# Kernel tuning notes

Measured on AMD Instinct MI355X. Metric: run time of the kernel, lower is better.

The kernel has to match this reference:

```python
import jax, jax.numpy as jnp
import numpy as np

B, S, D, MEM, STRIDE = 8, 8192, 128, 128, 64

def setup_inputs() -> dict:
    key = jax.random.key(0)
    ks = jax.random.split(key, 6)
    scale = 0.01  # matches nn.init.normal_(w, 0.0, 0.01)
    x = jax.random.normal(ks[0], (B, S, D), dtype=jnp.float32)
    Wq = scale * jax.random.normal(ks[1], (D, D), dtype=jnp.float32)
    Wk = scale * jax.random.normal(ks[2], (D, D), dtype=jnp.float32)
    Wv = scale * jax.random.normal(ks[3], (MEM, D), dtype=jnp.float32)
    Wg_w = jnp.zeros((1, D), dtype=jnp.float32)       # W_g weight init zeros
    Wg_b = jnp.full((1,), -2.0, dtype=jnp.float32)    # W_g bias init -2.0
    Wout = scale * jax.random.normal(ks[4], (D, MEM), dtype=jnp.float32)
    return {"x": x, "Wq": Wq, "Wk": Wk, "Wv": Wv, "Wg_w": Wg_w, "Wg_b": Wg_b, "Wout": Wout}

def reference(x, Wq, Wk, Wv, Wg_w, Wg_b, Wout):
    b, s, d = x.shape
    nC = s // STRIDE  # S assumed divisible by stride
    q = x @ Wq.T                                  # [B,S,D]
    k = x @ Wk.T                                  # [B,S,D]
    v = x @ Wv.T                                  # [B,S,MEM]
    g = jax.nn.sigmoid(x @ Wg_w.T + Wg_b)         # [B,S,1]
    # chunk: leading scan axis nC
    qc = q.reshape(b, nC, STRIDE, d).transpose(1, 0, 2, 3)
    kc = k.reshape(b, nC, STRIDE, d).transpose(1, 0, 2, 3)
    vc = v.reshape(b, nC, STRIDE, MEM).transpose(1, 0, 2, 3)
    gc = g.reshape(b, nC, STRIDE, 1).transpose(1, 0, 2, 3)

    def step(M, chunk):
        qch, kch, vch, gch = chunk
        reads = jnp.einsum('bsd,bdm->bsm', qch, M)              # read before write
        write = jnp.einsum('bsd,bsm->bdm', kch * gch, vch)      # gated outer-product
        avg_gate = gch.mean(axis=1, keepdims=True)              # [B,1,1]
        M_new = (1.0 - avg_gate) * M + write
        return M_new, reads

    M0 = jnp.zeros((b, d, MEM), dtype=x.dtype)
    _, reads = jax.lax.scan(step, M0, (qc, kc, vc, gc))         # [nC,B,STRIDE,MEM]
    out = reads.transpose(1, 0, 2, 3).reshape(b, s, MEM)
    return out @ Wout.T                                         # [B,S,D]
```

## Files before the change

kernel.cpp:

```cpp
#include <hip/hip_runtime.h>

#define Bn 8
#define Sn 8192
#define Dn 128
#define NCn 128

typedef _Float16 f16;
typedef f16 f16x2 __attribute__((ext_vector_type(2)));
typedef f16 f16x4 __attribute__((ext_vector_type(4)));
typedef float f32x4 __attribute__((ext_vector_type(4)));

static __device__ __forceinline__ f32x4 mfma16(f16x4 a, f16x4 b, f32x4 c) {
  return __builtin_amdgcn_mfma_f32_16x16x16f16(a, b, c, 0, 0, 0);
}

union UU { uint4 u; f16x2 h[4]; f16x4 q[2]; };


__global__ __launch_bounds__(64) void k_prep(
    const float* __restrict__ Wq, const float* __restrict__ Wk,
    const float* __restrict__ Wv, const float* __restrict__ Wout,
    f16* __restrict__ Amat, f16* __restrict__ r2) {
  const int blk = blockIdx.x;
  const int which = blk >> 6;
  const int t = blk & 63, ti = t >> 3, tj = t & 7;
  const int lane = threadIdx.x & 63, r16 = lane & 15, g4 = lane >> 4;
  f32x4 acc = {};
  if (which == 0) {
#pragma unroll
    for (int kk = 0; kk < 8; ++kk) {
      f16x4 af, bf;
#pragma unroll
      for (int j = 0; j < 4; ++j) {
        af[j] = (f16)Wq[(kk * 16 + g4 * 4 + j) * 128 + ti * 16 + r16];
        bf[j] = (f16)Wk[(kk * 16 + g4 * 4 + j) * 128 + tj * 16 + r16];
      }
      acc = mfma16(af, bf, acc);
    }
  } else {
#pragma unroll
    for (int kk = 0; kk < 8; ++kk) {
      f16x4 af, bf;
      float4 a4 = *(const float4*)(Wout + (ti * 16 + r16) * 128 + kk * 16 + g4 * 4);
      af[0] = (f16)a4.x; af[1] = (f16)a4.y; af[2] = (f16)a4.z; af[3] = (f16)a4.w;
#pragma unroll
      for (int j = 0; j < 4; ++j)
        bf[j] = (f16)Wv[(kk * 16 + g4 * 4 + j) * 128 + tj * 16 + r16];
      acc = mfma16(af, bf, acc);
    }
  }
  f16* dst = which ? r2 : Amat;
#pragma unroll
  for (int j = 0; j < 4; ++j)
    dst[(ti * 16 + g4 * 4 + j) * 128 + tj * 16 + r16] = (f16)acc[j];
}

__global__ __launch_bounds__(512, 8) void k_phase1(
    const float* __restrict__ x, const float* __restrict__ gw, const float* __restrict__ gb,
    const f16* __restrict__ Amat, const f16* __restrict__ r2,
    f16x4* __restrict__ wtg, float* __restrict__ gavg, f16* __restrict__ xh) {
  __shared__ __align__(16) f16 Xs[64][136];
  __shared__ __align__(16) f16x4 vP[2048];
  __shared__ float gs[64];
  const int h = blockIdx.x;
  const int grp = h & 127, m = h >> 7;
  const int b = grp >> 4, seg = grp & 15;
  const int c = seg * 8 + m;
  const int tid = threadIdx.x;
  {
    int s = tid >> 3, sub = tid & 7;
    const float* xrow = x + ((size_t)b * Sn + (size_t)c * 64 + s) * Dn;
    f16* xhrow = xh + (size_t)(b * NCn + c) * 8192 + s * 128;
    float gpart = 0.f;
#pragma unroll
    for (int i = 0; i < 4; ++i) {
      int col = sub * 4 + i * 32;
      float4 v = *(const float4*)(xrow + col);
      float4 g = *(const float4*)(gw + col);
      gpart += v.x * g.x + v.y * g.y + v.z * g.z + v.w * g.w;
      f16x4 hh = {(f16)v.x, (f16)v.y, (f16)v.z, (f16)v.w};
      *(f16x4*)&Xs[s][col] = hh;
      *(f16x4*)&xhrow[col] = hh;
    }
    gpart += __shfl_xor(gpart, 1);
    gpart += __shfl_xor(gpart, 2);
    gpart += __shfl_xor(gpart, 4);
    if (sub == 0) gs[s] = 1.f / (1.f + __expf(-(gpart + gb[0])));
  }
  __syncthreads();
  if (tid == 0) {
    float sum = 0.f;
#pragma unroll
    for (int i = 0; i < 64; ++i) sum += gs[i];
    gavg[b * NCn + c] = sum * (1.f / 64.f);
  }
  const int w = tid >> 6, lane = tid & 63, r16 = lane & 15, g4 = lane >> 4;
  f32x4 uacc[4] = {}, vacc[4] = {};
#pragma unroll
  for (int kk = 0; kk < 8; ++kk) {
    f16x4 bu = *(const f16x4*)&Amat[(w * 16 + r16) * 128 + kk * 16 + g4 * 4];
    f16x4 bv = *(const f16x4*)&r2[(w * 16 + r16) * 128 + kk * 16 + g4 * 4];
#pragma unroll
    for (int mr = 0; mr < 4; ++mr) {
      f16x4 af = *(f16x4*)&Xs[mr * 16 + r16][kk * 16 + g4 * 4];
      uacc[mr] = mfma16(af, bu, uacc[mr]);
      vacc[mr] = mfma16(af, bv, vacc[mr]);
    }
  }
  f16x4 ua[4];
#pragma unroll
  for (int mr = 0; mr < 4; ++mr) {
    float g0 = gs[mr * 16 + g4 * 4 + 0], g1 = gs[mr * 16 + g4 * 4 + 1];
    float g2 = gs[mr * 16 + g4 * 4 + 2], g3 = gs[mr * 16 + g4 * 4 + 3];
    f16x4 uh = {(f16)(uacc[mr][0] * g0), (f16)(uacc[mr][1] * g1),
                (f16)(uacc[mr][2] * g2), (f16)(uacc[mr][3] * g3)};
    ua[mr] = uh;
    f16x4 vh = {(f16)vacc[mr][0], (f16)vacc[mr][1], (f16)vacc[mr][2], (f16)vacc[mr][3]};
    vP[(mr * 8 + w) * 64 + lane] = vh;
  }
  __syncthreads();
  f32x4 z[8] = {};
#pragma unroll
  for (int ks = 0; ks < 4; ++ks)
#pragma unroll
    for (int ct = 0; ct < 8; ++ct)
      z[ct] = mfma16(ua[ks], vP[(ks * 8 + ct) * 64 + lane], z[ct]);
  f16x4* wdst = wtg + (size_t)(b * NCn + c) * 4096;
#pragma unroll
  for (int ct = 0; ct < 8; ++ct) {
    f16x4 zh = {(f16)z[ct][0], (f16)z[ct][1], (f16)z[ct][2], (f16)z[ct][3]};
    wdst[(w * 8 + ct) * 64 + lane] = zh;
  }
}

__global__ __launch_bounds__(512, 4) void k_outfold(
    const f16* __restrict__ xh, const uint4* __restrict__ wtg4,
    const float* __restrict__ gavg, float* __restrict__ outp) {
  __shared__ __align__(16) f16 Xs[64][136];
  __shared__ __align__(16) float Mf[4096];
  __shared__ __align__(16) f16x4 Mh4[1024];
  const int blk = blockIdx.x;
  const int seg = 15 - (blk >> 5);
  const int sub5 = blk & 31;
  const int b = sub5 >> 2, q = sub5 & 3;
  const int tid = threadIdx.x;
  const int w = tid >> 6, lane = tid & 63, r16 = lane & 15, g4 = lane >> 4;
  const int mr = w & 3, tq = w >> 2;

  const int lt = tid >> 5;
  const int gtile = (lt >> 1) * 8 + q * 2 + (lt & 1);
  const int slot = tid & 31;

  float4 P0 = {0.f, 0.f, 0.f, 0.f}, P1 = {0.f, 0.f, 0.f, 0.f};
  {
    const uint4* Zb = wtg4 + (size_t)(b * NCn) * 2048 + gtile * 32 + slot;
    const float* ga = gavg + b * NCn;
    const int nt = seg * 8;
#pragma unroll 4
    for (int t = 0; t < nt; ++t) {
      UU z; z.u = Zb[(size_t)t * 2048];
      float dd = 1.f - ga[t];
      P0.x = dd * P0.x + (float)z.h[0][0];
      P0.y = dd * P0.y + (float)z.h[0][1];
      P0.z = dd * P0.z + (float)z.h[1][0];
      P0.w = dd * P0.w + (float)z.h[1][1];
      P1.x = dd * P1.x + (float)z.h[2][0];
      P1.y = dd * P1.y + (float)z.h[2][1];
      P1.z = dd * P1.z + (float)z.h[3][0];
      P1.w = dd * P1.w + (float)z.h[3][1];
    }
  }
  float4* Mf4 = (float4*)Mf;
  Mf4[tid * 2] = P0;
  Mf4[tid * 2 + 1] = P1;

  float dseg[8];
#pragma unroll
  for (int t = 0; t < 8; ++t) dseg[t] = 1.f - gavg[b * NCn + seg * 8 + t];

  const uint4* Zseg = wtg4 + (size_t)(b * NCn + seg * 8) * 2048;
  const f16* xhseg = xh + (size_t)(b * NCn + seg * 8) * 8192;
  const int xrow = tid >> 3, xcol = (tid & 7) * 16;

  uint4 xa = ((const uint4*)xhseg)[tid * 2];
  uint4 xb2 = ((const uint4*)xhseg)[tid * 2 + 1];

  for (int m = 0; m < 8; ++m) {
    *(uint4*)&Xs[xrow][xcol] = xa;
    *(uint4*)&Xs[xrow][xcol + 8] = xb2;
#pragma unroll
    for (int h2 = 0; h2 < 2; ++h2) {
      float4 mv = Mf4[tid * 2 + h2];
      f16x4 hh = {(f16)mv.x, (f16)mv.y, (f16)mv.z, (f16)mv.w};
      Mh4[tid * 2 + h2] = hh;
    }
    __syncthreads();

    UU z;
    z.u = Zseg[(size_t)m * 2048 + gtile * 32 + slot];
    if (m < 7) {
      const uint4* xn = (const uint4*)(xhseg + (size_t)(m + 1) * 8192);
      xa = xn[tid * 2];
      xb2 = xn[tid * 2 + 1];
    }

    f32x4 acc = {};
#pragma unroll
    for (int kk = 0; kk < 8; ++kk) {
      f16x4 af = *(f16x4*)&Xs[mr * 16 + r16][kk * 16 + g4 * 4];
      f16x4 bf = Mh4[(kk * 2 + tq) * 64 + lane];
      acc = mfma16(af, bf, acc);
    }

    {
      float dd = dseg[m];
#pragma unroll
      for (int h2 = 0; h2 < 2; ++h2) {
        float4 mv = Mf4[tid * 2 + h2];
        mv.x = dd * mv.x + (float)z.h[2 * h2][0];
        mv.y = dd * mv.y + (float)z.h[2 * h2][1];
        mv.z = dd * mv.z + (float)z.h[2 * h2 + 1][0];
        mv.w = dd * mv.w + (float)z.h[2 * h2 + 1][1];
        Mf4[tid * 2 + h2] = mv;
      }
    }

    {
      const int c = seg * 8 + m;
      float* ob = outp + ((size_t)b * Sn + (size_t)c * 64 + mr * 16 + g4 * 4) * Dn +
                  (q * 2 + tq) * 16 + r16;
#pragma unroll
      for (int j = 0; j < 4; ++j) ob[(size_t)j * Dn] = acc[j];
    }
    __syncthreads();
  }
}

extern "C" void kernel_launch(void* const* d_in, const int* in_sizes, int n_in,
                              void* d_out, int out_size, void* d_ws, size_t ws_size,
                              hipStream_t stream) {
  const float* x = (const float*)d_in[0];
  const float* Wq = (const float*)d_in[1];
  const float* Wk = (const float*)d_in[2];
  const float* Wv = (const float*)d_in[3];
  const float* gw = (const float*)d_in[4];
  const float* gb = (const float*)d_in[5];
  const float* Wout = (const float*)d_in[6];

  char* ws = (char*)d_ws;
  f16* Amat = (f16*)(ws + 0);
  f16* r2 = (f16*)(ws + 32768);
  float* gavg = (float*)(ws + 65536);
  f16* wtg = (f16*)(ws + 69632);
  f16* xh = (f16*)(ws + 37556224);

  k_prep<<<dim3(128), dim3(64), 0, stream>>>(Wq, Wk, Wv, Wout, Amat, r2);
  k_phase1<<<dim3(Bn * NCn), dim3(512), 0, stream>>>(x, gw, gb, Amat, r2, (f16x4*)wtg,
                                                     gavg, xh);
  k_outfold<<<dim3(512), dim3(512), 0, stream>>>(xh, (const uint4*)wtg, gavg,
                                                 (float*)d_out);
}
```

Measured before the change: 62.56 us.

## Keep memory state in registers and double-buffer shared tiles in outfold

```diff
diff --git a/kernel.cpp b/kernel.cpp
--- a/kernel.cpp
+++ b/kernel.cpp
@@ -17,13 +17,15 @@
 union UU { uint4 u; f16x2 h[4]; f16x4 q[2]; };
 
 
-__global__ __launch_bounds__(64) void k_prep(
+__global__ __launch_bounds__(256) void k_prep(
     const float* __restrict__ Wq, const float* __restrict__ Wk,
     const float* __restrict__ Wv, const float* __restrict__ Wout,
     f16* __restrict__ Amat, f16* __restrict__ r2) {
   const int blk = blockIdx.x;
-  const int which = blk >> 6;
-  const int t = blk & 63, ti = t >> 3, tj = t & 7;
+  const int which = blk >> 4;
+  const int w = threadIdx.x >> 6;
+  const int t = (blk & 15) * 4 + w;
+  const int ti = t >> 3, tj = t & 7;
   const int lane = threadIdx.x & 63, r16 = lane & 15, g4 = lane >> 4;
   f32x4 acc = {};
   if (which == 0) {
@@ -63,8 +65,7 @@
   __shared__ __align__(16) f16x4 vP[2048];
   __shared__ float gs[64];
   const int h = blockIdx.x;
-  const int grp = h & 127, m = h >> 7;
-  const int b = grp >> 4, seg = grp & 15;
+  const int b = h & 7, seg = (h >> 3) & 15, m = h >> 7;
   const int c = seg * 8 + m;
   const int tid = threadIdx.x;
   {
@@ -136,43 +137,36 @@
 __global__ __launch_bounds__(512, 4) void k_outfold(
     const f16* __restrict__ xh, const uint4* __restrict__ wtg4,
     const float* __restrict__ gavg, float* __restrict__ outp) {
-  __shared__ __align__(16) f16 Xs[64][136];
-  __shared__ __align__(16) float Mf[4096];
-  __shared__ __align__(16) f16x4 Mh4[1024];
+  __shared__ __align__(16) f16 Xs[2][64][136];
+  __shared__ __align__(16) f16x4 Mh4[2][1024];
   const int blk = blockIdx.x;
-  const int seg = 15 - (blk >> 5);
-  const int sub5 = blk & 31;
-  const int b = sub5 >> 2, q = sub5 & 3;
+  const int b = blk & 7, q = (blk >> 3) & 3, seg = 15 - (blk >> 5);
   const int tid = threadIdx.x;
   const int w = tid >> 6, lane = tid & 63, r16 = lane & 15, g4 = lane >> 4;
   const int mr = w & 3, tq = w >> 2;
-
   const int lt = tid >> 5;
   const int gtile = (lt >> 1) * 8 + q * 2 + (lt & 1);
   const int slot = tid & 31;
 
-  float4 P0 = {0.f, 0.f, 0.f, 0.f}, P1 = {0.f, 0.f, 0.f, 0.f};
+  float4 M0 = {0.f, 0.f, 0.f, 0.f}, M1 = {0.f, 0.f, 0.f, 0.f};
   {
     const uint4* Zb = wtg4 + (size_t)(b * NCn) * 2048 + gtile * 32 + slot;
     const float* ga = gavg + b * NCn;
     const int nt = seg * 8;
-#pragma unroll 4
+#pragma unroll 8
     for (int t = 0; t < nt; ++t) {
       UU z; z.u = Zb[(size_t)t * 2048];
       float dd = 1.f - ga[t];
-      P0.x = dd * P0.x + (float)z.h[0][0];
-      P0.y = dd * P0.y + (float)z.h[0][1];
-      P0.z = dd * P0.z + (float)z.h[1][0];
-      P0.w = dd * P0.w + (float)z.h[1][1];
-      P1.x = dd * P1.x + (float)z.h[2][0];
-      P1.y = dd * P1.y + (float)z.h[2][1];
-      P1.z = dd * P1.z + (float)z.h[3][0];
-      P1.w = dd * P1.w + (float)z.h[3][1];
-    }
-  }
-  float4* Mf4 = (float4*)Mf;
-  Mf4[tid * 2] = P0;
-  Mf4[tid * 2 + 1] = P1;
+      M0.x = dd * M0.x + (float)z.h[0][0];
+      M0.y = dd * M0.y + (float)z.h[0][1];
+      M0.z = dd * M0.z + (float)z.h[1][0];
+      M0.w = dd * M0.w + (float)z.h[1][1];
+      M1.x = dd * M1.x + (float)z.h[2][0];
+      M1.y = dd * M1.y + (float)z.h[2][1];
+      M1.z = dd * M1.z + (float)z.h[3][0];
+      M1.w = dd * M1.w + (float)z.h[3][1];
+    }
+  }
 
   float dseg[8];
 #pragma unroll
@@ -185,15 +179,14 @@
   uint4 xa = ((const uint4*)xhseg)[tid * 2];
   uint4 xb2 = ((const uint4*)xhseg)[tid * 2 + 1];
 
+#pragma unroll
   for (int m = 0; m < 8; ++m) {
-    *(uint4*)&Xs[xrow][xcol] = xa;
-    *(uint4*)&Xs[xrow][xcol + 8] = xb2;
-#pragma unroll
-    for (int h2 = 0; h2 < 2; ++h2) {
-      float4 mv = Mf4[tid * 2 + h2];
-      f16x4 hh = {(f16)mv.x, (f16)mv.y, (f16)mv.z, (f16)mv.w};
-      Mh4[tid * 2 + h2] = hh;
-    }
+    f16(*Xsb)[136] = Xs[m & 1];
+    f16x4* Mh = Mh4[m & 1];
+    *(uint4*)&Xsb[xrow][xcol] = xa;
+    *(uint4*)&Xsb[xrow][xcol + 8] = xb2;
+    Mh[tid * 2] = (f16x4){(f16)M0.x, (f16)M0.y, (f16)M0.z, (f16)M0.w};
+    Mh[tid * 2 + 1] = (f16x4){(f16)M1.x, (f16)M1.y, (f16)M1.z, (f16)M1.w};
     __syncthreads();
 
     UU z;
@@ -207,22 +200,21 @@
     f32x4 acc = {};
 #pragma unroll
     for (int kk = 0; kk < 8; ++kk) {
-      f16x4 af = *(f16x4*)&Xs[mr * 16 + r16][kk * 16 + g4 * 4];
-      f16x4 bf = Mh4[(kk * 2 + tq) * 64 + lane];
+      f16x4 af = *(f16x4*)&Xsb[mr * 16 + r16][kk * 16 + g4 * 4];
+      f16x4 bf = Mh[(kk * 2 + tq) * 64 + lane];
       acc = mfma16(af, bf, acc);
     }
 
     {
       float dd = dseg[m];
-#pragma unroll
-      for (int h2 = 0; h2 < 2; ++h2) {
-        float4 mv = Mf4[tid * 2 + h2];
-        mv.x = dd * mv.x + (float)z.h[2 * h2][0];
-        mv.y = dd * mv.y + (float)z.h[2 * h2][1];
-        mv.z = dd * mv.z + (float)z.h[2 * h2 + 1][0];
-        mv.w = dd * mv.w + (float)z.h[2 * h2 + 1][1];
-        Mf4[tid * 2 + h2] = mv;
-      }
+      M0.x = dd * M0.x + (float)z.h[0][0];
+      M0.y = dd * M0.y + (float)z.h[0][1];
+      M0.z = dd * M0.z + (float)z.h[1][0];
+      M0.w = dd * M0.w + (float)z.h[1][1];
+      M1.x = dd * M1.x + (float)z.h[2][0];
+      M1.y = dd * M1.y + (float)z.h[2][1];
+      M1.z = dd * M1.z + (float)z.h[3][0];
+      M1.w = dd * M1.w + (float)z.h[3][1];
     }
 
     {
@@ -232,7 +224,6 @@
 #pragma unroll
       for (int j = 0; j < 4; ++j) ob[(size_t)j * Dn] = acc[j];
     }
-    __syncthreads();
   }
 }
 
@@ -254,7 +245,7 @@
   f16* wtg = (f16*)(ws + 69632);
   f16* xh = (f16*)(ws + 37556224);
 
-  k_prep<<<dim3(128), dim3(64), 0, stream>>>(Wq, Wk, Wv, Wout, Amat, r2);
+  k_prep<<<dim3(32), dim3(256), 0, stream>>>(Wq, Wk, Wv, Wout, Amat, r2);
   k_phase1<<<dim3(Bn * NCn), dim3(512), 0, stream>>>(x, gw, gb, Amat, r2, (f16x4*)wtg,
                                                      gavg, xh);
   k_outfold<<<dim3(512), dim3(512), 0, stream>>>(xh, (const uint4*)wtg, gavg,
```

After: 57.89 us. 7.5% less time.
